# Kernel tuning notes

Hardware: AMD Instinct MI355X
Metric: run time of the kernel (lower is better)

Reference implementation:

```python
import jax, jax.numpy as jnp
import numpy as np

B, N = 4, 4096


def setup_inputs() -> dict:
    key = jax.random.key(0)
    k1, k2, k3, k4 = jax.random.split(key, 4)
    xyz1 = jax.random.normal(k1, (B, N, 3), dtype=jnp.float32)
    xyz2 = jax.random.normal(k2, (B, N, 3), dtype=jnp.float32)
    nor1 = jax.random.normal(k3, (B, N, 3), dtype=jnp.float32)
    nor2 = jax.random.normal(k4, (B, N, 3), dtype=jnp.float32)
    return {"xyz1": xyz1, "xyz2": xyz2, "nor1": nor1, "nor2": nor2}


def _kernel_sum(xa, xb, na, nb):
    # sum_{i,j} exp(-||xa_i - xb_j||^2) * (na_i . nb_j)^2
    diff = xa[:, :, None, :] - xb[:, None, :, :]          # [B, Na, Nb, 3]
    S = jnp.sum(diff * diff, axis=-1)                      # squared distances
    D = jnp.einsum('bid,bjd->bij', na, nb)                 # normal dot products
    return jnp.sum(jnp.exp(-S) * (D * D))


def reference(xyz1, xyz2, nor1, nor2):
    kxx = _kernel_sum(xyz1, xyz1, nor1, nor1)
    kyy = _kernel_sum(xyz2, xyz2, nor2, nor2)
    kxy = _kernel_sum(xyz1, xyz2, nor1, nor2)
    return kxx + kyy - 2.0 * kxy
```

## Files before the change

### kernel.cpp

```cpp
#include <hip/hip_runtime.h>


typedef short bf16x8 __attribute__((ext_vector_type(8)));
typedef float f32x16 __attribute__((ext_vector_type(16)));
typedef float f32x2  __attribute__((ext_vector_type(2)));

#define NPTS 4096
#define BATCH 4
#define IBLK 128
#define JCHUNK 512
#define LOG2E 1.4426950408889634f

#define NXY  (BATCH * 32 * 8)
#define NSYM (BATCH * 36 * 4)
#define GRID_MAIN (NXY + 2 * NSYM)

#define RSTRIDE 65536
#define REG(side, form, mat, b) \
    (((((((side)*2 + (form))*2 + (mat))*BATCH) + (b))) * (size_t)RSTRIDE)
#define PARTIALS_OFF (32 * (size_t)RSTRIDE)

__constant__ unsigned char SU_TBL[36] = {
    0x00,0x01,0x02,0x03,0x04,0x05,0x06,0x07,
    0x11,0x12,0x13,0x14,0x15,0x16,0x17,
    0x22,0x23,0x24,0x25,0x26,0x27,
    0x33,0x34,0x35,0x36,0x37,
    0x44,0x45,0x46,0x47,
    0x55,0x56,0x57,
    0x66,0x67,
    0x77
};

static __device__ __forceinline__ short f2bf(float f) {
    unsigned u = __builtin_bit_cast(unsigned, f);
    unsigned r = u + 0x7fffu + ((u >> 16) & 1u);
    return (short)(r >> 16);
}
static __device__ __forceinline__ void split(float v, float& h, float& l) {
    unsigned u = __builtin_bit_cast(unsigned, v);
    unsigned rb = (u + 0x7fffu + ((u >> 16) & 1u)) & 0xffff0000u;
    h = __builtin_bit_cast(float, rb);
    l = v - h;
}

static __device__ __forceinline__ void encodeA(float x0, float x1, float x2,
                                               float n0, float n1, float n2,
                                               float fS[16], float fD[16]) {
    float s2 = fmaf(x2, x2, fmaf(x1, x1, x0 * x0));
    float gh, gl; split(-LOG2E * s2, gh, gl);
    float u0h,u0l,u1h,u1l,u2h,u2l;
    split(2.f*LOG2E*x0, u0h, u0l);
    split(2.f*LOG2E*x1, u1h, u1l);
    split(2.f*LOG2E*x2, u2h, u2l);
    fS[0]=gh;  fS[1]=gl;  fS[2]=1.f; fS[3]=1.f;
    fS[4]=u0h; fS[5]=u0h; fS[6]=u0l;
    fS[7]=u1h; fS[8]=u1h; fS[9]=u1l;
    fS[10]=u2h; fS[11]=u2h; fS[12]=u2l;
    fS[13]=0.f; fS[14]=0.f; fS[15]=0.f;
    float m0h,m0l,m1h,m1l,m2h,m2l;
    split(n0, m0h, m0l); split(n1, m1h, m1l); split(n2, m2h, m2l);
    fD[0]=m0h; fD[1]=m0h; fD[2]=m0l;
    fD[3]=m1h; fD[4]=m1h; fD[5]=m1l;
    fD[6]=m2h; fD[7]=m2h; fD[8]=m2l;
#pragma unroll
    for (int k = 9; k < 16; ++k) fD[k] = 0.f;
}

static __device__ __forceinline__ void encodeB(float x0, float x1, float x2,
                                               float n0, float n1, float n2,
                                               float fS[16], float fD[16]) {
    float s2 = fmaf(x2, x2, fmaf(x1, x1, x0 * x0));
    float gh, gl; split(-LOG2E * s2, gh, gl);
    float v0h,v0l,v1h,v1l,v2h,v2l;
    split(x0, v0h, v0l); split(x1, v1h, v1l); split(x2, v2h, v2l);
    fS[0]=1.f; fS[1]=1.f; fS[2]=gh;  fS[3]=gl;
    fS[4]=v0h; fS[5]=v0l; fS[6]=v0h;
    fS[7]=v1h; fS[8]=v1l; fS[9]=v1h;
    fS[10]=v2h; fS[11]=v2l; fS[12]=v2h;
    fS[13]=0.f; fS[14]=0.f; fS[15]=0.f;
    float m0h,m0l,m1h,m1l,m2h,m2l;
    split(n0, m0h, m0l); split(n1, m1h, m1l); split(n2, m2h, m2l);
    fD[0]=m0h; fD[1]=m0l; fD[2]=m0h;
    fD[3]=m1h; fD[4]=m1l; fD[5]=m1h;
    fD[6]=m2h; fD[7]=m2l; fD[8]=m2h;
#pragma unroll
    for (int k = 9; k < 16; ++k) fD[k] = 0.f;
}

static __device__ __forceinline__ void store_units(short* base, int u0, const float f[16]) {
    bf16x8 a, b;
#pragma unroll
    for (int k = 0; k < 8; ++k) { a[k] = f2bf(f[k]); b[k] = f2bf(f[k + 8]); }
    *(bf16x8*)&base[(size_t)u0 * 8] = a;
    *(bf16x8*)&base[((size_t)u0 + 32) * 8] = b;
}

__global__ __launch_bounds__(256)
void vf_encode(const float* __restrict__ xyz1, const float* __restrict__ xyz2,
               const float* __restrict__ nor1, const float* __restrict__ nor2,
               short* __restrict__ ws)
{
    int gid = blockIdx.x * 256 + threadIdx.x;
    int side = gid >> 14;
    int b    = (gid >> 12) & 3;
    int j    = gid & 4095;

    const float* px = side ? xyz2 : xyz1;
    const float* pn = side ? nor2 : nor1;
    size_t off = ((size_t)b * NPTS + j) * 3;
    float x0 = px[off], x1 = px[off+1], x2 = px[off+2];
    float n0 = pn[off], n1 = pn[off+1], n2 = pn[off+2];

    float fS[16], fD[16];
    int u0 = (j >> 5) * 64 + (j & 31);

    encodeA(x0, x1, x2, n0, n1, n2, fS, fD);
    store_units(ws + REG(side, 0, 0, b), u0, fS);
    store_units(ws + REG(side, 0, 1, b), u0, fD);
    encodeB(x0, x1, x2, n0, n1, n2, fS, fD);
    store_units(ws + REG(side, 1, 0, b), u0, fS);
    store_units(ws + REG(side, 1, 1, b), u0, fD);
}

static __device__ __forceinline__ void epi(const f32x16& aS, const f32x16& aD,
                                           f32x2& q0, f32x2& q1) {
#pragma unroll
    for (int e = 0; e < 16; e += 4) {
        f32x2 ex0, ex1, d0, d1;
        ex0[0] = __builtin_amdgcn_exp2f(aS[e+0]);
        ex0[1] = __builtin_amdgcn_exp2f(aS[e+1]);
        ex1[0] = __builtin_amdgcn_exp2f(aS[e+2]);
        ex1[1] = __builtin_amdgcn_exp2f(aS[e+3]);
        d0[0] = aD[e+0]; d0[1] = aD[e+1];
        d1[0] = aD[e+2]; d1[1] = aD[e+3];
        q0 = __builtin_elementwise_fma(ex0 * d0, d0, q0);
        q1 = __builtin_elementwise_fma(ex1 * d1, d1, q1);
    }
}

__global__ __launch_bounds__(256, 4)
void vf_main(short* __restrict__ ws)
{
    __shared__ short sBS[JCHUNK * 16];
    __shared__ short sBD[JCHUNK * 16];

    int blk = blockIdx.x;
    int term, b, ib, jc; float wgt;
    if (blk < NXY) {
        term = 2; int r = blk;
        b = r & 3; r >>= 2;
        ib = r & 31; r >>= 5;
        jc = r;
        wgt = -2.f;
    } else {
        int s = blk - NXY;
        term = (s < NSYM) ? 0 : 1;
        if (s >= NSYM) s -= NSYM;
        b = s & 3; s >>= 2;
        int sub = s & 3; s >>= 2;
        unsigned e = SU_TBL[s];
        int g = e >> 4, j5 = e & 15;
        ib = g * 4 + sub;
        jc = j5;
        wgt = (g == j5) ? 1.f : 2.f;
    }

    int sideA = (term == 1) ? 1 : 0;
    int sideB = (term == 0) ? 0 : 1;

    const short* aSp = ws + REG(sideA, 0, 0, b);
    const short* aDp = ws + REG(sideA, 0, 1, b);
    const short* bSp = ws + REG(sideB, 1, 0, b) + (size_t)jc * 1024 * 8;
    const short* bDp = ws + REG(sideB, 1, 1, b) + (size_t)jc * 1024 * 8;

    const int tid  = threadIdx.x;
    const int lane = tid & 63;
    const int wv   = tid >> 6;

#pragma unroll
    for (int k = 0; k < 4; ++k) {
        int ul = tid + k * 256;
        *(bf16x8*)&sBS[(size_t)ul * 8] = *(const bf16x8*)&bSp[(size_t)ul * 8];
        *(bf16x8*)&sBD[(size_t)ul * 8] = *(const bf16x8*)&bDp[(size_t)ul * 8];
    }

    int ua = (ib * 4 + wv) * 64 + lane;
    bf16x8 AS = *(const bf16x8*)&aSp[(size_t)ua * 8];
    bf16x8 AD = *(const bf16x8*)&aDp[(size_t)ua * 8];

    __syncthreads();

    f32x16 z;
#pragma unroll
    for (int k = 0; k < 16; ++k) z[k] = 0.f;

    f32x2 q0 = {0.f, 0.f}, q1 = {0.f, 0.f};

#pragma unroll
    for (int jt = 0; jt < JCHUNK / 32; ++jt) {
        int u = (jt * 64 + lane) * 8;
        bf16x8 BS = *(const bf16x8*)&sBS[u];
        bf16x8 BD = *(const bf16x8*)&sBD[u];
        f32x16 aSacc = __builtin_amdgcn_mfma_f32_32x32x16_bf16(AS, BS, z, 0, 0, 0);
        f32x16 aDacc = __builtin_amdgcn_mfma_f32_32x32x16_bf16(AD, BD, z, 0, 0, 0);
        epi(aSacc, aDacc, q0, q1);
    }

    float part = (q0[0] + q0[1]) + (q1[0] + q1[1]);
#pragma unroll
    for (int off = 32; off > 0; off >>= 1)
        part += __shfl_down(part, off, 64);

    __syncthreads();
    float* red = (float*)sBS;
    if (lane == 0) red[wv] = part;
    __syncthreads();
    if (tid == 0) {
        float s = (red[0] + red[1]) + (red[2] + red[3]);
        float* partials = (float*)(ws + PARTIALS_OFF);
        partials[blk] = wgt * s;
    }
}

__global__ __launch_bounds__(256)
void vf_reduce(const short* __restrict__ ws, float* __restrict__ out)
{
    const float* partials = (const float*)(ws + PARTIALS_OFF);
    int tid = threadIdx.x;
    double s = 0.0;
#pragma unroll
    for (int k = 0; k < (GRID_MAIN + 255) / 256; ++k) {
        int idx = tid + k * 256;
        if (idx < GRID_MAIN) s += (double)partials[idx];
    }
#pragma unroll
    for (int off = 32; off > 0; off >>= 1)
        s += __shfl_down(s, off, 64);
    __shared__ double red[4];
    int lane = tid & 63, wv = tid >> 6;
    if (lane == 0) red[wv] = s;
    __syncthreads();
    if (tid == 0)
        out[0] = (float)((red[0] + red[1]) + (red[2] + red[3]));
}

extern "C" void kernel_launch(void* const* d_in, const int* in_sizes, int n_in,
                              void* d_out, int out_size, void* d_ws, size_t ws_size,
                              hipStream_t stream) {
    const float* xyz1 = (const float*)d_in[0];
    const float* xyz2 = (const float*)d_in[1];
    const float* nor1 = (const float*)d_in[2];
    const float* nor2 = (const float*)d_in[3];
    float* out = (float*)d_out;
    short* ws  = (short*)d_ws;

    vf_encode<<<(2 * BATCH * NPTS) / 256, 256, 0, stream>>>(xyz1, xyz2, nor1, nor2, ws);
    vf_main<<<GRID_MAIN, 256, 0, stream>>>(ws);
    vf_reduce<<<1, 256, 0, stream>>>(ws, out);
}
```

Before: 86.62 us.

## Fuse final reduction into main kernel via atomic counter and drop LDS staging

Removes the separate reduce launch by having the last finishing block, detected through an atomic counter reset in the encode kernel, sum all partials. Also replaces shared-memory staging of the B chunk with direct per-wave global loads and one-step register prefetch, which eliminates the barrier and LDS usage. The trade-off is that each wave now reads B redundantly from global/L2 memory, and the counter adds atomics and fences.

```diff
diff --git a/kernel.cpp b/kernel.cpp
--- a/kernel.cpp
+++ b/kernel.cpp
@@ -19,6 +19,7 @@
 #define REG(side, form, mat, b) \
     (((((((side)*2 + (form))*2 + (mat))*BATCH) + (b))) * (size_t)RSTRIDE)
 #define PARTIALS_OFF (32 * (size_t)RSTRIDE)
+#define COUNTER_OFF  (PARTIALS_OFF + 8192)
 
 __constant__ unsigned char SU_TBL[36] = {
     0x00,0x01,0x02,0x03,0x04,0x05,0x06,0x07,
@@ -105,6 +106,8 @@
     int b    = (gid >> 12) & 3;
     int j    = gid & 4095;
 
+    if (gid == 0) *(unsigned*)&ws[COUNTER_OFF] = 0u;
+
     const float* px = side ? xyz2 : xyz1;
     const float* pn = side ? nor2 : nor1;
     size_t off = ((size_t)b * NPTS + j) * 3;
@@ -139,11 +142,8 @@
 }
 
 __global__ __launch_bounds__(256, 4)
-void vf_main(short* __restrict__ ws)
+void vf_main(short* __restrict__ ws, float* __restrict__ out)
 {
-    __shared__ short sBS[JCHUNK * 16];
-    __shared__ short sBD[JCHUNK * 16];
-
     int blk = blockIdx.x;
     int term, b, ib, jc; float wgt;
     if (blk < NXY) {
@@ -177,33 +177,31 @@
     const int lane = tid & 63;
     const int wv   = tid >> 6;
 
-#pragma unroll
-    for (int k = 0; k < 4; ++k) {
-        int ul = tid + k * 256;
-        *(bf16x8*)&sBS[(size_t)ul * 8] = *(const bf16x8*)&bSp[(size_t)ul * 8];
-        *(bf16x8*)&sBD[(size_t)ul * 8] = *(const bf16x8*)&bDp[(size_t)ul * 8];
-    }
-
     int ua = (ib * 4 + wv) * 64 + lane;
     bf16x8 AS = *(const bf16x8*)&aSp[(size_t)ua * 8];
     bf16x8 AD = *(const bf16x8*)&aDp[(size_t)ua * 8];
 
-    __syncthreads();
-
     f32x16 z;
 #pragma unroll
     for (int k = 0; k < 16; ++k) z[k] = 0.f;
 
     f32x2 q0 = {0.f, 0.f}, q1 = {0.f, 0.f};
 
+    bf16x8 BS = *(const bf16x8*)&bSp[(size_t)lane * 8];
+    bf16x8 BD = *(const bf16x8*)&bDp[(size_t)lane * 8];
+
 #pragma unroll
     for (int jt = 0; jt < JCHUNK / 32; ++jt) {
-        int u = (jt * 64 + lane) * 8;
-        bf16x8 BS = *(const bf16x8*)&sBS[u];
-        bf16x8 BD = *(const bf16x8*)&sBD[u];
+        bf16x8 nBS = BS, nBD = BD;
+        if (jt + 1 < JCHUNK / 32) {
+            size_t u = ((size_t)(jt + 1) * 64 + lane) * 8;
+            nBS = *(const bf16x8*)&bSp[u];
+            nBD = *(const bf16x8*)&bDp[u];
+        }
         f32x16 aSacc = __builtin_amdgcn_mfma_f32_32x32x16_bf16(AS, BS, z, 0, 0, 0);
         f32x16 aDacc = __builtin_amdgcn_mfma_f32_32x32x16_bf16(AD, BD, z, 0, 0, 0);
         epi(aSacc, aDacc, q0, q1);
+        BS = nBS; BD = nBD;
     }
 
     float part = (q0[0] + q0[1]) + (q1[0] + q1[1]);
@@ -211,37 +209,38 @@
     for (int off = 32; off > 0; off >>= 1)
         part += __shfl_down(part, off, 64);
 
-    __syncthreads();
-    float* red = (float*)sBS;
+    __shared__ float red[4];
+    __shared__ int lastflag;
     if (lane == 0) red[wv] = part;
     __syncthreads();
     if (tid == 0) {
         float s = (red[0] + red[1]) + (red[2] + red[3]);
-        float* partials = (float*)(ws + PARTIALS_OFF);
+        float* partials = (float*)&ws[PARTIALS_OFF];
         partials[blk] = wgt * s;
-    }
-}
-
-__global__ __launch_bounds__(256)
-void vf_reduce(const short* __restrict__ ws, float* __restrict__ out)
-{
-    const float* partials = (const float*)(ws + PARTIALS_OFF);
-    int tid = threadIdx.x;
-    double s = 0.0;
-#pragma unroll
-    for (int k = 0; k < (GRID_MAIN + 255) / 256; ++k) {
-        int idx = tid + k * 256;
-        if (idx < GRID_MAIN) s += (double)partials[idx];
-    }
-#pragma unroll
-    for (int off = 32; off > 0; off >>= 1)
-        s += __shfl_down(s, off, 64);
-    __shared__ double red[4];
-    int lane = tid & 63, wv = tid >> 6;
-    if (lane == 0) red[wv] = s;
+        __threadfence();
+        unsigned old = atomicAdd((unsigned*)&ws[COUNTER_OFF], 1u);
+        lastflag = (old == GRID_MAIN - 1) ? 1 : 0;
+    }
     __syncthreads();
-    if (tid == 0)
-        out[0] = (float)((red[0] + red[1]) + (red[2] + red[3]));
+
+    if (lastflag) {
+        __threadfence();
+        const float* partials = (const float*)&ws[PARTIALS_OFF];
+        double s = 0.0;
+#pragma unroll
+        for (int k = 0; k < (GRID_MAIN + 255) / 256; ++k) {
+            int idx = tid + k * 256;
+            if (idx < GRID_MAIN) s += (double)partials[idx];
+        }
+#pragma unroll
+        for (int off = 32; off > 0; off >>= 1)
+            s += __shfl_down(s, off, 64);
+        __shared__ double dred[4];
+        if (lane == 0) dred[wv] = s;
+        __syncthreads();
+        if (tid == 0)
+            out[0] = (float)((dred[0] + dred[1]) + (dred[2] + dred[3]));
+    }
 }
 
 extern "C" void kernel_launch(void* const* d_in, const int* in_sizes, int n_in,
@@ -255,6 +254,5 @@
     short* ws  = (short*)d_ws;
 
     vf_encode<<<(2 * BATCH * NPTS) / 256, 256, 0, stream>>>(xyz1, xyz2, nor1, nor2, ws);
-    vf_main<<<GRID_MAIN, 256, 0, stream>>>(ws);
-    vf_reduce<<<1, 256, 0, stream>>>(ws, out);
-}
+    vf_main<<<GRID_MAIN, 256, 0, stream>>>(ws, out);
+}
```

Measured after the change: 116.0 us. 34.0% more time.

## Exploit tile-level symmetry inside diagonal blocks of self-kernel sums

Applied to the files above, without the earlier changes.

Self-term diagonal 512x512 blocks now compute only the upper-triangular 32x32 tiles. Diagonal tiles get weight 1 and off-diagonal tiles weight 2. Each wave pairs row tiles r and 15-r so every wave does the same number of tiles. This removes about half of the redundant MFMA and exp work on diagonal blocks and shrinks the grid. The cost is wave-uniform branching inside the unrolled loop and more register pressure from holding two A fragments.

```diff
diff --git a/kernel.cpp b/kernel.cpp
--- a/kernel.cpp
+++ b/kernel.cpp
@@ -7,28 +7,27 @@
 
 #define NPTS 4096
 #define BATCH 4
-#define IBLK 128
 #define JCHUNK 512
 #define LOG2E 1.4426950408889634f
 
-#define NXY  (BATCH * 32 * 8)
-#define NSYM (BATCH * 36 * 4)
-#define GRID_MAIN (NXY + 2 * NSYM)
+#define NDIAG (2 * BATCH * 8 * 2)
+#define NOFF  (2 * BATCH * 28 * 4)
+#define NXY   (BATCH * 32 * 8)
+#define GRID_MAIN (NDIAG + NOFF + NXY)
 
 #define RSTRIDE 65536
 #define REG(side, form, mat, b) \
     (((((((side)*2 + (form))*2 + (mat))*BATCH) + (b))) * (size_t)RSTRIDE)
 #define PARTIALS_OFF (32 * (size_t)RSTRIDE)
 
-__constant__ unsigned char SU_TBL[36] = {
-    0x00,0x01,0x02,0x03,0x04,0x05,0x06,0x07,
-    0x11,0x12,0x13,0x14,0x15,0x16,0x17,
-    0x22,0x23,0x24,0x25,0x26,0x27,
-    0x33,0x34,0x35,0x36,0x37,
-    0x44,0x45,0x46,0x47,
-    0x55,0x56,0x57,
-    0x66,0x67,
-    0x77
+__constant__ unsigned char OFF_TBL[28] = {
+    0x01,0x02,0x03,0x04,0x05,0x06,0x07,
+    0x12,0x13,0x14,0x15,0x16,0x17,
+    0x23,0x24,0x25,0x26,0x27,
+    0x34,0x35,0x36,0x37,
+    0x45,0x46,0x47,
+    0x56,0x57,
+    0x67
 };
 
 static __device__ __forceinline__ short f2bf(float f) {
@@ -145,24 +144,40 @@
     __shared__ short sBD[JCHUNK * 16];
 
     int blk = blockIdx.x;
-    int term, b, ib, jc; float wgt;
-    if (blk < NXY) {
-        term = 2; int r = blk;
-        b = r & 3; r >>= 2;
-        ib = r & 31; r >>= 5;
-        jc = r;
+    const int tid  = threadIdx.x;
+    const int lane = tid & 63;
+    const int wv   = tid >> 6;
+
+    int term, b, jc;
+    int isdiag = 0;
+    int ib = 0;
+    int g = 0, job = 0;
+    float wgt = 0.f;
+
+    if (blk < NDIAG) {
+        isdiag = 1;
+        int d = blk;
+        term = d >> 6; d &= 63;
+        b = d & 3; d >>= 2;
+        g = d & 7; job = d >> 3;
+        jc = g;
+    } else if (blk < NDIAG + NOFF) {
+        int o = blk - NDIAG;
+        term = (o < NOFF / 2) ? 0 : 1;
+        if (term) o -= NOFF / 2;
+        b = o & 3; o >>= 2;
+        int sub = o & 3; int st = o >> 2;
+        unsigned e = OFF_TBL[st];
+        ib = (e >> 4) * 4 + sub;
+        jc = e & 15;
+        wgt = 2.f;
+    } else {
+        int x = blk - (NDIAG + NOFF);
+        term = 2;
+        b = x & 3; x >>= 2;
+        ib = x & 31;
+        jc = x >> 5;
         wgt = -2.f;
-    } else {
-        int s = blk - NXY;
-        term = (s < NSYM) ? 0 : 1;
-        if (s >= NSYM) s -= NSYM;
-        b = s & 3; s >>= 2;
-        int sub = s & 3; s >>= 2;
-        unsigned e = SU_TBL[s];
-        int g = e >> 4, j5 = e & 15;
-        ib = g * 4 + sub;
-        jc = j5;
-        wgt = (g == j5) ? 1.f : 2.f;
     }
 
     int sideA = (term == 1) ? 1 : 0;
@@ -173,10 +188,6 @@
     const short* bSp = ws + REG(sideB, 1, 0, b) + (size_t)jc * 1024 * 8;
     const short* bDp = ws + REG(sideB, 1, 1, b) + (size_t)jc * 1024 * 8;
 
-    const int tid  = threadIdx.x;
-    const int lane = tid & 63;
-    const int wv   = tid >> 6;
-
 #pragma unroll
     for (int k = 0; k < 4; ++k) {
         int ul = tid + k * 256;
@@ -184,29 +195,65 @@
         *(bf16x8*)&sBD[(size_t)ul * 8] = *(const bf16x8*)&bDp[(size_t)ul * 8];
     }
 
-    int ua = (ib * 4 + wv) * 64 + lane;
-    bf16x8 AS = *(const bf16x8*)&aSp[(size_t)ua * 8];
-    bf16x8 AD = *(const bf16x8*)&aDp[(size_t)ua * 8];
-
-    __syncthreads();
-
     f32x16 z;
 #pragma unroll
     for (int k = 0; k < 16; ++k) z[k] = 0.f;
 
     f32x2 q0 = {0.f, 0.f}, q1 = {0.f, 0.f};
-
-#pragma unroll
-    for (int jt = 0; jt < JCHUNK / 32; ++jt) {
-        int u = (jt * 64 + lane) * 8;
-        bf16x8 BS = *(const bf16x8*)&sBS[u];
-        bf16x8 BD = *(const bf16x8*)&sBD[u];
-        f32x16 aSacc = __builtin_amdgcn_mfma_f32_32x32x16_bf16(AS, BS, z, 0, 0, 0);
-        f32x16 aDacc = __builtin_amdgcn_mfma_f32_32x32x16_bf16(AD, BD, z, 0, 0, 0);
-        epi(aSacc, aDacc, q0, q1);
-    }
-
-    float part = (q0[0] + q0[1]) + (q1[0] + q1[1]);
+    f32x2 p0 = {0.f, 0.f}, p1 = {0.f, 0.f};
+    float part;
+
+    if (!isdiag) {
+        int ua = (ib * 4 + wv) * 64 + lane;
+        bf16x8 AS = *(const bf16x8*)&aSp[(size_t)ua * 8];
+        bf16x8 AD = *(const bf16x8*)&aDp[(size_t)ua * 8];
+
+        __syncthreads();
+
+#pragma unroll
+        for (int jt = 0; jt < JCHUNK / 32; ++jt) {
+            int u = (jt * 64 + lane) * 8;
+            bf16x8 BS = *(const bf16x8*)&sBS[u];
+            bf16x8 BD = *(const bf16x8*)&sBD[u];
+            f32x16 aSacc = __builtin_amdgcn_mfma_f32_32x32x16_bf16(AS, BS, z, 0, 0, 0);
+            f32x16 aDacc = __builtin_amdgcn_mfma_f32_32x32x16_bf16(AD, BD, z, 0, 0, 0);
+            epi(aSacc, aDacc, q0, q1);
+        }
+        part = wgt * ((q0[0] + q0[1]) + (q1[0] + q1[1]));
+    } else {
+        int r   = job * 4 + wv;
+        int rt1 = r, rt2 = 15 - r;
+        int ua1 = (g * 16 + rt1) * 64 + lane;
+        int ua2 = (g * 16 + rt2) * 64 + lane;
+        bf16x8 AS1 = *(const bf16x8*)&aSp[(size_t)ua1 * 8];
+        bf16x8 AD1 = *(const bf16x8*)&aDp[(size_t)ua1 * 8];
+        bf16x8 AS2 = *(const bf16x8*)&aSp[(size_t)ua2 * 8];
+        bf16x8 AD2 = *(const bf16x8*)&aDp[(size_t)ua2 * 8];
+
+        __syncthreads();
+
+#pragma unroll
+        for (int jt = 0; jt < JCHUNK / 32; ++jt) {
+            int u = (jt * 64 + lane) * 8;
+            bf16x8 BS = *(const bf16x8*)&sBS[u];
+            bf16x8 BD = *(const bf16x8*)&sBD[u];
+            if (jt >= rt1) {
+                f32x16 aS = __builtin_amdgcn_mfma_f32_32x32x16_bf16(AS1, BS, z, 0, 0, 0);
+                f32x16 aD = __builtin_amdgcn_mfma_f32_32x32x16_bf16(AD1, BD, z, 0, 0, 0);
+                if (jt == rt1) epi(aS, aD, p0, p1);
+                else           epi(aS, aD, q0, q1);
+            }
+            if (jt >= rt2) {
+                f32x16 aS = __builtin_amdgcn_mfma_f32_32x32x16_bf16(AS2, BS, z, 0, 0, 0);
+                f32x16 aD = __builtin_amdgcn_mfma_f32_32x32x16_bf16(AD2, BD, z, 0, 0, 0);
+                if (jt == rt2) epi(aS, aD, p0, p1);
+                else           epi(aS, aD, q0, q1);
+            }
+        }
+        part = ((p0[0] + p0[1]) + (p1[0] + p1[1]))
+             + 2.f * ((q0[0] + q0[1]) + (q1[0] + q1[1]));
+    }
+
 #pragma unroll
     for (int off = 32; off > 0; off >>= 1)
         part += __shfl_down(part, off, 64);
@@ -218,7 +265,7 @@
     if (tid == 0) {
         float s = (red[0] + red[1]) + (red[2] + red[3]);
         float* partials = (float*)(ws + PARTIALS_OFF);
-        partials[blk] = wgt * s;
+        partials[blk] = s;
     }
 }
 
```

New measurement: 81.64 us. 5.7% less time.
